# Kernel tuning notes

Hardware: AMD Instinct MI355X
Metric: run time of the kernel (lower is better)

## Reference

```python
import jax, jax.numpy as jnp
import numpy as np

TOKENS_PER_LAYER = 16  # v in rearrange 'b l (a v) -> b l a v'


def setup_inputs() -> dict:
    key = jax.random.key(0)
    k1, k2 = jax.random.split(key)
    vocab, embed_dim = 1024, 256
    x = jax.random.normal(k1, (64, 32, embed_dim * TOKENS_PER_LAYER), dtype=jnp.float32)
    # nn.Embedding init: uniform(-1/vocab, 1/vocab)
    emb_weight = jax.random.uniform(k2, (vocab, embed_dim), dtype=jnp.float32,
                                    minval=-1.0 / vocab, maxval=1.0 / vocab)
    return {"x": x, "emb_weight": emb_weight}


def reference(x, emb_weight):
    v = TOKENS_PER_LAYER
    b, l, av = x.shape
    a = av // v  # embed_dim
    # rearrange 'b l (a v) -> b l a v'
    z = x.reshape(b, l, a, v)
    # rearrange 'b l a v -> (b l v) a'
    z_flat = z.transpose(0, 1, 3, 2).reshape(b * l * v, a)
    # pairwise squared L2 distance via sum-of-squares + GEMM: [N, vocab]
    dist = (jnp.sum(z_flat * z_flat, axis=1, keepdims=True)
            + jnp.sum(emb_weight * emb_weight, axis=1)
            - 2.0 * (z_flat @ emb_weight.T))
    tokens = jnp.argmin(dist, axis=-1)  # [N] int
    # embedding gather, then rearrange '(b l v) e -> b l e v'
    z_q = emb_weight[tokens].reshape(b, l, v, a).transpose(0, 1, 3, 2)
    # straight-through decoder input: z + sg(z_q - z)
    decoder_input = z + jax.lax.stop_gradient(z_q - z)
    tokens = tokens.reshape(b, l, v)
    return z_q, decoder_input, tokens
```

## Files before the change

### kernel.cpp

```cpp
#include <hip/hip_runtime.h>


#define A_DIM 256
#define VOCAB 1024
#define NROWS 32768
#define ZQ_ELEMS ((size_t)8388608)
#define TAU_C 3.0e-4f
#define TAU_F 2.0e-4f

typedef _Float16 f16x8 __attribute__((ext_vector_type(8)));
typedef float f32x4 __attribute__((ext_vector_type(4)));

#define WS_EHT   ((size_t)0)
#define WS_ZH    ((size_t)524288)
#define WS_ESQ   ((size_t)17301504)
#define WS_ZSQ   ((size_t)17305600)
#define WS_QRES  ((size_t)17436672)
#define WS_TOK   ((size_t)20582400)
#define WS_PLIST ((size_t)20713472)
#define WS_FLIST ((size_t)21237760)
#define WS_CNT   ((size_t)21368832)
#define WS_NEED  ((size_t)21368960)

__device__ __forceinline__ void async_copy16(const void* g, void* l) {
    __builtin_amdgcn_global_load_lds(
        (const __attribute__((address_space(1))) unsigned int*)g,
        (__attribute__((address_space(3))) unsigned int*)l, 16, 0, 0);
}


__global__ __launch_bounds__(256) void prep_e_kernel(const float* __restrict__ emb,
                                                     float* __restrict__ esq,
                                                     _Float16* __restrict__ eht,
                                                     int* __restrict__ cnt) {
    int j = blockIdx.x * 256 + threadIdx.x;
    if (blockIdx.x == 0 && threadIdx.x < 2) cnt[threadIdx.x] = 0;
    if (j >= VOCAB) return;
    const float4* row = (const float4*)(emb + (size_t)j * A_DIM);
    double s = 0.0;
    #pragma unroll 4
    for (int t = 0; t < A_DIM / 4; ++t) {
        float4 f = row[t];
        float sx = f.x * f.x, sy = f.y * f.y, sz = f.z * f.z, sw = f.w * f.w;
        s += (double)sx + (double)sy + (double)sz + (double)sw;
    }
    esq[j] = (float)s;
    #pragma unroll 4
    for (int kb = 0; kb < 32; ++kb) {
        float4 e0 = row[kb * 2], e1 = row[kb * 2 + 1];
        f16x8 h;
        h[0] = (_Float16)e0.x; h[1] = (_Float16)e0.y; h[2] = (_Float16)e0.z; h[3] = (_Float16)e0.w;
        h[4] = (_Float16)e1.x; h[5] = (_Float16)e1.y; h[6] = (_Float16)e1.z; h[7] = (_Float16)e1.w;
        *(f16x8*)(eht + ((size_t)kb * 1024 + j) * 8) = h;
    }
}

__global__ __launch_bounds__(256) void prep_z_kernel(const float* __restrict__ x,
                                                     _Float16* __restrict__ zh,
                                                     float* __restrict__ zsq) {
    __shared__ float raw[A_DIM * 17];
    const int tid = threadIdx.x;
    const int bl = blockIdx.x;
    #pragma unroll
    for (int t = 0; t < 4; ++t) {
        int f4 = tid * 4 + t * 1024;
        float4 val = *(const float4*)(x + (size_t)bl * 4096 + f4);
        int a = f4 >> 4, v0 = f4 & 15;
        raw[a * 17 + v0 + 0] = val.x;
        raw[a * 17 + v0 + 1] = val.y;
        raw[a * 17 + v0 + 2] = val.z;
        raw[a * 17 + v0 + 3] = val.w;
    }
    __syncthreads();
    #pragma unroll
    for (int t = 0; t < 16; ++t) {
        int f = tid + t * 256;
        int v = f >> 8, a = f & 255;
        zh[((size_t)bl * 16 + v) * 256 + a] = (_Float16)raw[a * 17 + v];
    }
    if (tid < 16) {
        double s = 0.0;
        for (int a = 0; a < A_DIM; ++a) {
            float zf = raw[a * 17 + tid];
            float z2 = zf * zf;
            s += (double)z2;
        }
        zsq[bl * 16 + tid] = (float)s;
    }
}

__global__ __launch_bounds__(256, 4) void mfma_kernel(const _Float16* __restrict__ zh,
                                                      const _Float16* __restrict__ eht,
                                                      const float* __restrict__ esq_g,
                                                      float* __restrict__ qres) {
    __shared__ __align__(16) _Float16 lb[2][32 * 32 * 8];
    const int tid = threadIdx.x;
    const int w = tid >> 6;
    const int lane = tid & 63;
    const int q = lane >> 4;
    const int ln = lane & 15;

    const int wg = blockIdx.x;
    const int j = wg >> 3;
    const int rowblk = (wg & 7) * 64 + (j >> 2);
    const int quarter = j & 3;
    const int row0 = rowblk * 64 + w * 16;
    const int cq0 = quarter * 256;

    {
        #pragma unroll
        for (int t = 0; t < 4; ++t) {
            int f = tid + t * 256;
            const _Float16* gsrc = eht + ((size_t)(f >> 5) * 1024 + cq0 + (f & 31)) * 8;
            _Float16* ldst = &lb[0][(size_t)(t * 256 + w * 64) * 8];
            async_copy16(gsrc, ldst);
        }
    }

    f16x8 afr[8];
    #pragma unroll
    for (int kt = 0; kt < 8; ++kt)
        afr[kt] = *(const f16x8*)(zh + (size_t)(row0 + ln) * 256 + kt * 32 + q * 8);

    float tv1[4], tv2[4], tv3[4];
    int   ti1[4], ti2[4], ti3[4];
    #pragma unroll
    for (int s = 0; s < 4; ++s) {
        tv1[s] = 3.0e38f; tv2[s] = 3.0e38f; tv3[s] = 3.0e38f;
        ti1[s] = 0; ti2[s] = 0; ti3[s] = 0;
    }

    for (int chunk = 0; chunk < 8; ++chunk) {
        const int b = chunk & 1;
        asm volatile("s_waitcnt vmcnt(0)" ::: "memory");
        __syncthreads();
        if (chunk + 1 < 8) {
            const int cb = cq0 + (chunk + 1) * 32;
            #pragma unroll
            for (int t = 0; t < 4; ++t) {
                int f = tid + t * 256;
                const _Float16* gsrc = eht + ((size_t)(f >> 5) * 1024 + cb + (f & 31)) * 8;
                _Float16* ldst = &lb[b ^ 1][(size_t)(t * 256 + w * 64) * 8];
                async_copy16(gsrc, ldst);
            }
        }

        f32x4 acc[2];
        #pragma unroll
        for (int nt = 0; nt < 2; ++nt)
            acc[nt] = (f32x4){0.f, 0.f, 0.f, 0.f};

        #pragma unroll
        for (int kt = 0; kt < 8; ++kt) {
            #pragma unroll
            for (int nt = 0; nt < 2; ++nt) {
                f16x8 bfr = *(const f16x8*)&lb[b][((size_t)(kt * 4 + q) * 32 + nt * 16 + ln) * 8];
                acc[nt] = __builtin_amdgcn_mfma_f32_16x16x32_f16(afr[kt], bfr, acc[nt], 0, 0, 0);
            }
        }

        #pragma unroll
        for (int nt = 0; nt < 2; ++nt) {
            int c = cq0 + chunk * 32 + nt * 16 + ln;
            float es = esq_g[c];
            #pragma unroll
            for (int reg = 0; reg < 4; ++reg) {
                float s = fmaf(-2.0f, acc[nt][reg], es);
                if (s < tv3[reg]) {
                    if (s < tv2[reg]) {
                        tv3[reg] = tv2[reg]; ti3[reg] = ti2[reg];
                        if (s < tv1[reg]) {
                            tv2[reg] = tv1[reg]; ti2[reg] = ti1[reg];
                            tv1[reg] = s; ti1[reg] = c;
                        } else { tv2[reg] = s; ti2[reg] = c; }
                    } else { tv3[reg] = s; ti3[reg] = c; }
                }
            }
        }
    }

    #pragma unroll
    for (int slot = 0; slot < 4; ++slot) {
        float v1 = tv1[slot], v2 = tv2[slot], v3 = tv3[slot];
        int i1 = ti1[slot], i2 = ti2[slot], i3 = ti3[slot];
        #pragma unroll
        for (int m = 1; m <= 8; m <<= 1) {
            float ov1 = __shfl_xor(v1, m); int oi1 = __shfl_xor(i1, m);
            float ov2 = __shfl_xor(v2, m); int oi2 = __shfl_xor(i2, m);
            float ov3 = __shfl_xor(v3, m); int oi3 = __shfl_xor(i3, m);
            #define INS3(ov, oi)                                                         \
                if (ov < v3 || (ov == v3 && oi < i3)) {                                  \
                    if (ov < v2 || (ov == v2 && oi < i2)) {                              \
                        v3 = v2; i3 = i2;                                                \
                        if (ov < v1 || (ov == v1 && oi < i1)) {                          \
                            v2 = v1; i2 = i1; v1 = ov; i1 = oi;                          \
                        } else { v2 = ov; i2 = oi; }                                     \
                    } else { v3 = ov; i3 = oi; }                                         \
                }
            INS3(ov1, oi1)
            INS3(ov2, oi2)
            INS3(ov3, oi3)
            #undef INS3
        }
        if (ln == 0) {
            int row = row0 + q * 4 + slot;
            float* hp = qres + ((size_t)row * 4 + quarter) * 6;
            hp[0] = v1; hp[1] = __int_as_float(i1);
            hp[2] = v2; hp[3] = __int_as_float(i2);
            hp[4] = v3; hp[5] = __int_as_float(i3);
        }
    }
}

__global__ __launch_bounds__(256) void finalize_kernel(const float* __restrict__ qres,
                                                       int* __restrict__ tok,
                                                       int4* __restrict__ plist,
                                                       int* __restrict__ flist,
                                                       int* __restrict__ cnt,
                                                       float* __restrict__ out) {
    int row = blockIdx.x * 256 + threadIdx.x;
    const float* h0 = qres + (size_t)row * 24;
    float v1 = h0[0]; int i1 = __float_as_int(h0[1]);
    float v2 = h0[2]; int i2 = __float_as_int(h0[3]);
    float v3 = h0[4]; int i3 = __float_as_int(h0[5]);
    #pragma unroll
    for (int e = 0; e < 9; ++e) {
        float ov = h0[6 + 2 * e]; int oi = __float_as_int(h0[7 + 2 * e]);
        if (ov < v3 || (ov == v3 && oi < i3)) {
            if (ov < v2 || (ov == v2 && oi < i2)) {
                v3 = v2; i3 = i2;
                if (ov < v1 || (ov == v1 && oi < i1)) {
                    v2 = v1; i2 = i1; v1 = ov; i1 = oi;
                } else { v2 = ov; i2 = oi; }
            } else { v3 = ov; i3 = oi; }
        }
    }
    tok[row] = i1;
    out[2 * ZQ_ELEMS + (size_t)row] = (float)i1;
    if (v2 - v1 <= TAU_C) {
        if (v3 - v1 > TAU_C) {
            int p = atomicAdd(&cnt[0], 1);
            plist[p] = make_int4(row, i1, i2, 0);
        } else {
            int p = atomicAdd(&cnt[1], 1);
            flist[p] = row;
        }
    }
}

__global__ __launch_bounds__(256) void rescan2_kernel(const float* __restrict__ x,
                                                      const float* __restrict__ emb,
                                                      const float* __restrict__ esq,
                                                      const float* __restrict__ zsq,
                                                      int* __restrict__ tok,
                                                      const int4* __restrict__ plist,
                                                      const int* __restrict__ flist,
                                                      const int* __restrict__ cnt,
                                                      float* __restrict__ out) {
    __shared__ float zrow[A_DIM];
    __shared__ float wv[4];
    __shared__ int   wi[4];
    const int tid = threadIdx.x;
    const int w = tid >> 6, lane = tid & 63;

    {
        const int nw = gridDim.x * 4;
        const int gw = blockIdx.x * 4 + w;
        const int np = cnt[0];
        for (int i = gw; i < np; i += nw) {
            int4 e = plist[i];
            const int r = e.x, c1 = e.y, c2 = e.z;
            const float* xr = x + (size_t)(r >> 4) * 4096 + (r & 15);
            const float* e1 = emb + (size_t)c1 * A_DIM;
            const float* e2 = emb + (size_t)c2 * A_DIM;
            double d1 = 0.0, d2 = 0.0;
            #pragma unroll
            for (int k = 0; k < 4; ++k) {
                int a = lane + k * 64;
                double zv = (double)xr[a * 16];
                d1 = fma(zv, (double)e1[a], d1);
                d2 = fma(zv, (double)e2[a], d2);
            }
            #pragma unroll
            for (int m = 1; m < 64; m <<= 1) {
                d1 += __shfl_xor(d1, m);
                d2 += __shfl_xor(d2, m);
            }
            if (lane == 0) {
                float zq = zsq[r];
                float A1 = zq + esq[c1];
                float D1 = (float)(2.0 * d1);
                float s1 = A1 - D1;
                float A2 = zq + esq[c2];
                float D2 = (float)(2.0 * d2);
                float s2 = A2 - D2;
                int bi = (s2 < s1 || (s2 == s1 && c2 < c1)) ? c2 : c1;
                tok[r] = bi;
                out[2 * ZQ_ELEMS + (size_t)r] = (float)bi;
            }
        }
    }

    const int nf = cnt[1];
    for (int i = blockIdx.x; i < nf; i += gridDim.x) {
        const int r = flist[i];
        __syncthreads();
        zrow[tid] = x[(size_t)(r >> 4) * 4096 + (size_t)tid * 16 + (r & 15)];
        __syncthreads();

        const float4* e0 = (const float4*)(emb + (size_t)tid * 4 * A_DIM);
        double d0 = 0.0, d1 = 0.0, d2 = 0.0, d3 = 0.0;
        #pragma unroll 8
        for (int k4 = 0; k4 < A_DIM / 4; ++k4) {
            float4 zf = *(const float4*)&zrow[k4 * 4];
            double z0 = (double)zf.x, z1 = (double)zf.y;
            double z2 = (double)zf.z, z3 = (double)zf.w;
            float4 f0 = e0[k4];
            float4 f1 = e0[64 + k4];
            float4 f2 = e0[128 + k4];
            float4 f3 = e0[192 + k4];
            d0 = fma((double)f0.x, z0, d0); d0 = fma((double)f0.y, z1, d0);
            d0 = fma((double)f0.z, z2, d0); d0 = fma((double)f0.w, z3, d0);
            d1 = fma((double)f1.x, z0, d1); d1 = fma((double)f1.y, z1, d1);
            d1 = fma((double)f1.z, z2, d1); d1 = fma((double)f1.w, z3, d1);
            d2 = fma((double)f2.x, z0, d2); d2 = fma((double)f2.y, z1, d2);
            d2 = fma((double)f2.z, z2, d2); d2 = fma((double)f2.w, z3, d2);
            d3 = fma((double)f3.x, z0, d3); d3 = fma((double)f3.y, z1, d3);
            d3 = fma((double)f3.z, z2, d3); d3 = fma((double)f3.w, z3, d3);
        }
        const float zq = zsq[r];
        float bv = 3.0e38f; int bi = 0;
        double dd[4] = {d0, d1, d2, d3};
        #pragma unroll
        for (int cc = 0; cc < 4; ++cc) {
            int c = tid * 4 + cc;
            float A = zq + esq[c];
            float D = (float)(2.0 * dd[cc]);
            float s = A - D;
            if (s < bv) { bv = s; bi = c; }
        }
        #pragma unroll
        for (int m = 1; m < 64; m <<= 1) {
            float ov = __shfl_xor(bv, m); int oi = __shfl_xor(bi, m);
            if (ov < bv || (ov == bv && oi < bi)) { bv = ov; bi = oi; }
        }
        if (lane == 0) { wv[w] = bv; wi[w] = bi; }
        __syncthreads();
        if (tid == 0) {
            float BV = wv[0]; int BI = wi[0];
            #pragma unroll
            for (int t = 1; t < 4; ++t)
                if (wv[t] < BV || (wv[t] == BV && wi[t] < BI)) { BV = wv[t]; BI = wi[t]; }
            tok[r] = BI;
            out[2 * ZQ_ELEMS + (size_t)r] = (float)BI;
        }
    }
}

__global__ __launch_bounds__(256) void gather_kernel(const float* __restrict__ emb,
                                                     const int* __restrict__ tok,
                                                     float* __restrict__ out) {
    __shared__ int t16[16];
    const int tid = threadIdx.x;
    const int bl = blockIdx.x;
    if (tid < 16) t16[tid] = tok[bl * 16 + tid];
    __syncthreads();
    const int a = tid;
    __align__(16) float h[16];
    #pragma unroll
    for (int v = 0; v < 16; ++v) h[v] = emb[(size_t)t16[v] * A_DIM + a];
    size_t base = ((size_t)bl * A_DIM + a) * 16;
    float4* p0 = (float4*)(out + base);
    float4* p1 = (float4*)(out + ZQ_ELEMS + base);
    #pragma unroll
    for (int qq = 0; qq < 4; ++qq) {
        float4 val = *(float4*)&h[qq * 4];
        p0[qq] = val;
        p1[qq] = val;
    }
}


__global__ __launch_bounds__(256) void prep_f(const float* __restrict__ emb,
                                              float* __restrict__ e_sq32) {
    int j = blockIdx.x * 256 + threadIdx.x;
    if (j < VOCAB) {
        const float4* row = (const float4*)(emb + (size_t)j * A_DIM);
        double s = 0.0;
        #pragma unroll 4
        for (int t = 0; t < A_DIM / 4; ++t) {
            float4 f = row[t];
            float sx = f.x * f.x, sy = f.y * f.y, sz = f.z * f.z, sw = f.w * f.w;
            s += (double)sx + (double)sy + (double)sz + (double)sw;
        }
        e_sq32[j] = (float)s;
    }
}

#define FBM 64
#define FBN 256
#define FBK 32
struct SmemF {
    union {
        struct { float zs[FBK][FBM]; float es[FBK][FBN]; };
        float4 mbuf[FBM][32];
        struct { double zrow[A_DIM]; float rbest[256]; int ridx[256]; };
    };
    double zsqp_s[4][FBM];
    float  zsq[FBM];
    int    tok[FBM];
    int    flagrows[FBM];
    int    nflag;
};

__global__ __launch_bounds__(256, 2) void main_f(const float* __restrict__ x,
                                                 const float* __restrict__ emb,
                                                 const float* __restrict__ e_sq32,
                                                 float* __restrict__ out) {
    __shared__ SmemF sm;
    const int tid = threadIdx.x;
    const int tx = tid & 31;
    const int ty = tid >> 5;
    const int blk = blockIdx.x;
    const int row0 = blk * FBM;
    const int bl0 = row0 >> 4;
    const int zrow_id = tid & 63;
    const int zq4     = tid >> 6;

    if (tid == 0) sm.nflag = 0;
    float v1[8], v2[8];
    int   i1[8], i2[8];
    #pragma unroll
    for (int r = 0; r < 8; ++r) { v1[r] = 3.0e38f; v2[r] = 3.0e38f; i1[r] = 0; i2[r] = 0; }
    double zsqp = 0.0;
    float4 zpf[2];
    float4 epf[8];
    for (int ct = 0; ct < VOCAB / FBN; ++ct) {
        float acc[8][8];
        #pragma unroll
        for (int rr = 0; rr < 8; ++rr)
            #pragma unroll
            for (int cc = 0; cc < 8; ++cc) acc[rr][cc] = 0.0f;
        for (int kt = 0; kt < A_DIM / FBK; ++kt) {
            if (kt == 0) {
                #pragma unroll
                for (int t = 0; t < 2; ++t) {
                    int f = tid + t * 256;
                    int v4 = f & 3, g = (f >> 2) & 3, kk = f >> 4;
                    zpf[t] = *(const float4*)(x + (size_t)(bl0 + g) * 4096 + (kt * FBK + kk) * 16 + v4 * 4);
                }
                #pragma unroll
                for (int t = 0; t < 8; ++t) {
                    int f = tid + t * 256;
                    int c = f & 255, k4 = f >> 8;
                    epf[t] = *(const float4*)(emb + (size_t)(ct * FBN + c) * A_DIM + kt * FBK + k4 * 4);
                }
            }
            __syncthreads();
            #pragma unroll
            for (int t = 0; t < 2; ++t) {
                int f = tid + t * 256;
                int v4 = f & 3, g = (f >> 2) & 3, kk = f >> 4;
                *(float4*)&sm.zs[kk][g * 16 + v4 * 4] = zpf[t];
            }
            #pragma unroll
            for (int t = 0; t < 8; ++t) {
                int f = tid + t * 256;
                int c = f & 255, k4 = f >> 8;
                sm.es[k4 * 4 + 0][c] = epf[t].x;
                sm.es[k4 * 4 + 1][c] = epf[t].y;
                sm.es[k4 * 4 + 2][c] = epf[t].z;
                sm.es[k4 * 4 + 3][c] = epf[t].w;
            }
            __syncthreads();
            if (kt + 1 < A_DIM / FBK) {
                #pragma unroll
                for (int t = 0; t < 2; ++t) {
                    int f = tid + t * 256;
                    int v4 = f & 3, g = (f >> 2) & 3, kk = f >> 4;
                    zpf[t] = *(const float4*)(x + (size_t)(bl0 + g) * 4096 + ((kt + 1) * FBK + kk) * 16 + v4 * 4);
                }
                #pragma unroll
                for (int t = 0; t < 8; ++t) {
                    int f = tid + t * 256;
                    int c = f & 255, k4 = f >> 8;
                    epf[t] = *(const float4*)(emb + (size_t)(ct * FBN + c) * A_DIM + (kt + 1) * FBK + k4 * 4);
                }
            }
            if (ct == 0 && (kt >> 1) == zq4) {
                #pragma unroll
                for (int kk = 0; kk < FBK; ++kk) {
                    float zf = sm.zs[kk][zrow_id];
                    float zf2 = zf * zf;
                    zsqp += (double)zf2;
                }
            }
            #pragma unroll 2
            for (int kk = 0; kk < FBK; ++kk) {
                float4 za = *(float4*)&sm.zs[kk][ty * 4];
                float4 zb = *(float4*)&sm.zs[kk][32 + ty * 4];
                float4 ea = *(float4*)&sm.es[kk][tx * 4];
                float4 eb = *(float4*)&sm.es[kk][128 + tx * 4];
                float zv[8] = {za.x, za.y, za.z, za.w, zb.x, zb.y, zb.z, zb.w};
                float ev[8] = {ea.x, ea.y, ea.z, ea.w, eb.x, eb.y, eb.z, eb.w};
                #pragma unroll
                for (int rr = 0; rr < 8; ++rr)
                    #pragma unroll
                    for (int cc = 0; cc < 8; ++cc)
                        acc[rr][cc] = fmaf(zv[rr], ev[cc], acc[rr][cc]);
            }
        }
        if (ct == 0) {
            sm.zsqp_s[zq4][zrow_id] = zsqp;
            __syncthreads();
            if (tid < FBM)
                sm.zsq[tid] = (float)(sm.zsqp_s[0][tid] + sm.zsqp_s[1][tid]
                                    + sm.zsqp_s[2][tid] + sm.zsqp_s[3][tid]);
            __syncthreads();
        }
        float esqv[8];
        #pragma unroll
        for (int cc = 0; cc < 8; ++cc) {
            int c = ct * FBN + (cc >> 2) * 128 + tx * 4 + (cc & 3);
            esqv[cc] = e_sq32[c];
        }
        #pragma unroll
        for (int rr = 0; rr < 8; ++rr) {
            int R = (rr >> 2) * 32 + ty * 4 + (rr & 3);
            float zq = sm.zsq[R];
            #pragma unroll
            for (int cc = 0; cc < 8; ++cc) {
                int c = ct * FBN + (cc >> 2) * 128 + tx * 4 + (cc & 3);
                float A = zq + esqv[cc];
                float s = fmaf(-2.0f, acc[rr][cc], A);
                if (s < v1[rr]) { v2[rr] = v1[rr]; i2[rr] = i1[rr]; v1[rr] = s; i1[rr] = c; }
                else if (s < v2[rr]) { v2[rr] = s; i2[rr] = c; }
            }
        }
    }
    __syncthreads();
    #pragma unroll
    for (int rr = 0; rr < 8; ++rr) {
        int r = (rr >> 2) * 32 + ty * 4 + (rr & 3);
        float4 m;
        m.x = v1[rr]; m.y = __int_as_float(i1[rr]);
        m.z = v2[rr]; m.w = __int_as_float(i2[rr]);
        sm.mbuf[r][tx] = m;
    }
    __syncthreads();
    if (tid < FBM) {
        int r = tid;
        float V1 = 3.0e38f, V2 = 3.0e38f;
        int I1 = 0, I2 = 0;
        for (int t = 0; t < 32; ++t) {
            float4 m = sm.mbuf[r][t];
            float a1 = m.x; int a1i = __float_as_int(m.y);
            float a2 = m.z; int a2i = __float_as_int(m.w);
            if (a1 < V1 || (a1 == V1 && a1i < I1)) { V2 = V1; I2 = I1; V1 = a1; I1 = a1i; }
            else if (a1 < V2 || (a1 == V2 && a1i < I2)) { V2 = a1; I2 = a1i; }
            if (a2 < V1 || (a2 == V1 && a2i < I1)) { V2 = V1; I2 = I1; V1 = a2; I1 = a2i; }
            else if (a2 < V2 || (a2 == V2 && a2i < I2)) { V2 = a2; I2 = a2i; }
        }
        sm.tok[r] = I1;
        if (V2 - V1 <= TAU_F) {
            int pos = atomicAdd(&sm.nflag, 1);
            sm.flagrows[pos] = r;
        }
    }
    __syncthreads();
    const int nf = sm.nflag;
    for (int i = 0; i < nf; ++i) {
        const int rl = sm.flagrows[i];
        const int bl = bl0 + (rl >> 4);
        const int v  = rl & 15;
        const float zqrow = sm.zsq[rl];
        sm.zrow[tid] = (double)x[(size_t)bl * 4096 + (size_t)tid * 16 + v];
        __syncthreads();
        float bv = 3.0e38f; int bi = 0;
        #pragma unroll
        for (int cc = 0; cc < 4; ++cc) {
            int c = tid * 4 + cc;
            const float4* er = (const float4*)(emb + (size_t)c * A_DIM);
            double dot = 0.0;
            #pragma unroll 8
            for (int k4 = 0; k4 < A_DIM / 4; ++k4) {
                float4 f = er[k4];
                dot = fma((double)f.x, sm.zrow[k4 * 4 + 0], dot);
                dot = fma((double)f.y, sm.zrow[k4 * 4 + 1], dot);
                dot = fma((double)f.z, sm.zrow[k4 * 4 + 2], dot);
                dot = fma((double)f.w, sm.zrow[k4 * 4 + 3], dot);
            }
            float A = zqrow + e_sq32[c];
            float D = (float)(2.0 * dot);
            float s = A - D;
            if (s < bv) { bv = s; bi = c; }
        }
        sm.rbest[tid] = bv; sm.ridx[tid] = bi;
        __syncthreads();
        if (tid == 0) {
            float BV = sm.rbest[0]; int BI = sm.ridx[0];
            for (int t = 1; t < 256; ++t) {
                float vv = sm.rbest[t];
                if (vv < BV) { BV = vv; BI = sm.ridx[t]; }
            }
            sm.tok[rl] = BI;
        }
        __syncthreads();
    }
    if (tid < FBM) {
        out[2 * ZQ_ELEMS + (size_t)(row0 + tid)] = (float)sm.tok[tid];
    }
    __syncthreads();
    const int a = tid;
    for (int g = 0; g < 4; ++g) {
        __align__(16) float h[16];
        #pragma unroll
        for (int v = 0; v < 16; ++v) {
            h[v] = emb[(size_t)sm.tok[g * 16 + v] * A_DIM + a];
        }
        size_t base = ((size_t)(bl0 + g) * A_DIM + a) * 16;
        float4* p0 = (float4*)(out + base);
        float4* p1 = (float4*)(out + ZQ_ELEMS + base);
        #pragma unroll
        for (int qq = 0; qq < 4; ++qq) {
            float4 val = *(float4*)&h[qq * 4];
            p0[qq] = val;
            p1[qq] = val;
        }
    }
}

extern "C" void kernel_launch(void* const* d_in, const int* in_sizes, int n_in,
                              void* d_out, int out_size, void* d_ws, size_t ws_size,
                              hipStream_t stream) {
    (void)in_sizes; (void)n_in; (void)out_size;
    const float* x   = (const float*)d_in[0];
    const float* emb = (const float*)d_in[1];
    float* out = (float*)d_out;
    char* ws = (char*)d_ws;

    if (ws_size >= WS_NEED) {
        _Float16* eht = (_Float16*)(ws + WS_EHT);
        _Float16* zh  = (_Float16*)(ws + WS_ZH);
        float* esq    = (float*)(ws + WS_ESQ);
        float* zsq    = (float*)(ws + WS_ZSQ);
        float* qres   = (float*)(ws + WS_QRES);
        int* tok      = (int*)(ws + WS_TOK);
        int4* plist   = (int4*)(ws + WS_PLIST);
        int* flist    = (int*)(ws + WS_FLIST);
        int* cnt      = (int*)(ws + WS_CNT);

        prep_e_kernel<<<4, 256, 0, stream>>>(emb, esq, eht, cnt);
        prep_z_kernel<<<2048, 256, 0, stream>>>(x, zh, zsq);
        mfma_kernel<<<2048, 256, 0, stream>>>(zh, eht, esq, qres);
        finalize_kernel<<<128, 256, 0, stream>>>(qres, tok, plist, flist, cnt, out);
        rescan2_kernel<<<256, 256, 0, stream>>>(x, emb, esq, zsq, tok, plist, flist, cnt, out);
        gather_kernel<<<2048, 256, 0, stream>>>(emb, tok, out);
    } else {
        float* e_sq32 = (float*)ws;
        prep_f<<<4, 256, 0, stream>>>(emb, e_sq32);
        main_f<<<512, 256, 0, stream>>>(x, emb, e_sq32, out);
    }
}
```

Before: 250.5 us.

## Fuse finalize into MFMA kernel with full-vocab scan per block and register double-buffering

The MFMA kernel now scans all 1024 codebook entries per row block instead of splitting the vocabulary into quarters across blocks. It writes tokens and the ambiguous-row lists directly, which removes the partial-result buffer and the separate finalize kernel launch. B fragments are loaded straight from global memory into registers with two-way double buffering, replacing the LDS async-copy pipeline and its barriers. The trade-off is a grid of 512 blocks with lower occupancy (launch bounds 256,2) and a longer serial loop per wave, which may expose global load latency.

```diff
diff --git a/kernel.cpp b/kernel.cpp
--- a/kernel.cpp
+++ b/kernel.cpp
@@ -15,18 +15,11 @@
 #define WS_ZH    ((size_t)524288)
 #define WS_ESQ   ((size_t)17301504)
 #define WS_ZSQ   ((size_t)17305600)
-#define WS_QRES  ((size_t)17436672)
-#define WS_TOK   ((size_t)20582400)
-#define WS_PLIST ((size_t)20713472)
-#define WS_FLIST ((size_t)21237760)
-#define WS_CNT   ((size_t)21368832)
-#define WS_NEED  ((size_t)21368960)
-
-__device__ __forceinline__ void async_copy16(const void* g, void* l) {
-    __builtin_amdgcn_global_load_lds(
-        (const __attribute__((address_space(1))) unsigned int*)g,
-        (__attribute__((address_space(3))) unsigned int*)l, 16, 0, 0);
-}
+#define WS_TOK   ((size_t)17436672)
+#define WS_PLIST ((size_t)17567744)
+#define WS_FLIST ((size_t)18092032)
+#define WS_CNT   ((size_t)18223104)
+#define WS_NEED  ((size_t)18223232)
 
 
 __global__ __launch_bounds__(256) void prep_e_kernel(const float* __restrict__ emb,
@@ -89,33 +82,20 @@
     }
 }
 
-__global__ __launch_bounds__(256, 4) void mfma_kernel(const _Float16* __restrict__ zh,
+__global__ __launch_bounds__(256, 2) void mfma_kernel(const _Float16* __restrict__ zh,
                                                       const _Float16* __restrict__ eht,
                                                       const float* __restrict__ esq_g,
-                                                      float* __restrict__ qres) {
-    __shared__ __align__(16) _Float16 lb[2][32 * 32 * 8];
+                                                      int* __restrict__ tok,
+                                                      int4* __restrict__ plist,
+                                                      int* __restrict__ flist,
+                                                      int* __restrict__ cnt,
+                                                      float* __restrict__ out) {
     const int tid = threadIdx.x;
     const int w = tid >> 6;
     const int lane = tid & 63;
     const int q = lane >> 4;
     const int ln = lane & 15;
-
-    const int wg = blockIdx.x;
-    const int j = wg >> 3;
-    const int rowblk = (wg & 7) * 64 + (j >> 2);
-    const int quarter = j & 3;
-    const int row0 = rowblk * 64 + w * 16;
-    const int cq0 = quarter * 256;
-
-    {
-        #pragma unroll
-        for (int t = 0; t < 4; ++t) {
-            int f = tid + t * 256;
-            const _Float16* gsrc = eht + ((size_t)(f >> 5) * 1024 + cq0 + (f & 31)) * 8;
-            _Float16* ldst = &lb[0][(size_t)(t * 256 + w * 64) * 8];
-            async_copy16(gsrc, ldst);
-        }
-    }
+    const int row0 = blockIdx.x * 64 + w * 16;
 
     f16x8 afr[8];
     #pragma unroll
@@ -130,54 +110,48 @@
         ti1[s] = 0; ti2[s] = 0; ti3[s] = 0;
     }
 
-    for (int chunk = 0; chunk < 8; ++chunk) {
-        const int b = chunk & 1;
-        asm volatile("s_waitcnt vmcnt(0)" ::: "memory");
-        __syncthreads();
-        if (chunk + 1 < 8) {
-            const int cb = cq0 + (chunk + 1) * 32;
-            #pragma unroll
-            for (int t = 0; t < 4; ++t) {
-                int f = tid + t * 256;
-                const _Float16* gsrc = eht + ((size_t)(f >> 5) * 1024 + cb + (f & 31)) * 8;
-                _Float16* ldst = &lb[b ^ 1][(size_t)(t * 256 + w * 64) * 8];
-                async_copy16(gsrc, ldst);
-            }
-        }
-
-        f32x4 acc[2];
-        #pragma unroll
-        for (int nt = 0; nt < 2; ++nt)
-            acc[nt] = (f32x4){0.f, 0.f, 0.f, 0.f};
-
-        #pragma unroll
-        for (int kt = 0; kt < 8; ++kt) {
-            #pragma unroll
-            for (int nt = 0; nt < 2; ++nt) {
-                f16x8 bfr = *(const f16x8*)&lb[b][((size_t)(kt * 4 + q) * 32 + nt * 16 + ln) * 8];
-                acc[nt] = __builtin_amdgcn_mfma_f32_16x16x32_f16(afr[kt], bfr, acc[nt], 0, 0, 0);
-            }
-        }
-
-        #pragma unroll
-        for (int nt = 0; nt < 2; ++nt) {
-            int c = cq0 + chunk * 32 + nt * 16 + ln;
-            float es = esq_g[c];
-            #pragma unroll
-            for (int reg = 0; reg < 4; ++reg) {
-                float s = fmaf(-2.0f, acc[nt][reg], es);
-                if (s < tv3[reg]) {
-                    if (s < tv2[reg]) {
-                        tv3[reg] = tv2[reg]; ti3[reg] = ti2[reg];
-                        if (s < tv1[reg]) {
-                            tv2[reg] = tv1[reg]; ti2[reg] = ti1[reg];
-                            tv1[reg] = s; ti1[reg] = c;
-                        } else { tv2[reg] = s; ti2[reg] = c; }
-                    } else { tv3[reg] = s; ti3[reg] = c; }
-                }
-            }
-        }
-    }
+    #define LOAD_CHUNK(c0, bfr)                                                          \
+        {                                                                                \
+            _Pragma("unroll")                                                            \
+            for (int kt = 0; kt < 8; ++kt)                                               \
+                bfr[kt] = *(const f16x8*)(eht +                                          \
+                    ((size_t)(kt * 4 + q) * 1024 + (c0) + ln) * 8);                      \
+        }
+
+    #define COMPUTE_CHUNK(c0, bfr)                                                       \
+        {                                                                                \
+            f32x4 acc = (f32x4){0.f, 0.f, 0.f, 0.f};                                     \
+            _Pragma("unroll")                                                            \
+            for (int kt = 0; kt < 8; ++kt)                                               \
+                acc = __builtin_amdgcn_mfma_f32_16x16x32_f16(afr[kt], bfr[kt], acc,      \
+                                                             0, 0, 0);                   \
+            const int cand = (c0) + ln;                                                  \
+            float es = esq_g[cand];                                                      \
+            _Pragma("unroll")                                                            \
+            for (int reg = 0; reg < 4; ++reg) {                                          \
+                float s = fmaf(-2.0f, acc[reg], es);                                     \
+                if (s < tv3[reg]) {                                                      \
+                    if (s < tv2[reg]) {                                                  \
+                        tv3[reg] = tv2[reg]; ti3[reg] = ti2[reg];                        \
+                        if (s < tv1[reg]) {                                              \
+                            tv2[reg] = tv1[reg]; ti2[reg] = ti1[reg];                    \
+                            tv1[reg] = s; ti1[reg] = cand;                               \
+                        } else { tv2[reg] = s; ti2[reg] = cand; }                        \
+                    } else { tv3[reg] = s; ti3[reg] = cand; }                            \
+                }                                                                        \
+            }                                                                            \
+        }
+
+    f16x8 bA[8], bB[8];
+    LOAD_CHUNK(0, bA)
+    for (int ch = 0; ch < 64; ch += 2) {
+        LOAD_CHUNK((ch + 1) * 16, bB)
+        COMPUTE_CHUNK(ch * 16, bA)
+        if (ch + 2 < 64) LOAD_CHUNK((ch + 2) * 16, bA)
+        COMPUTE_CHUNK((ch + 1) * 16, bB)
+    }
+    #undef LOAD_CHUNK
+    #undef COMPUTE_CHUNK
 
     #pragma unroll
     for (int slot = 0; slot < 4; ++slot) {
@@ -204,46 +178,17 @@
         }
         if (ln == 0) {
             int row = row0 + q * 4 + slot;
-            float* hp = qres + ((size_t)row * 4 + quarter) * 6;
-            hp[0] = v1; hp[1] = __int_as_float(i1);
-            hp[2] = v2; hp[3] = __int_as_float(i2);
-            hp[4] = v3; hp[5] = __int_as_float(i3);
-        }
-    }
-}
-
-__global__ __launch_bounds__(256) void finalize_kernel(const float* __restrict__ qres,
-                                                       int* __restrict__ tok,
-                                                       int4* __restrict__ plist,
-                                                       int* __restrict__ flist,
-                                                       int* __restrict__ cnt,
-                                                       float* __restrict__ out) {
-    int row = blockIdx.x * 256 + threadIdx.x;
-    const float* h0 = qres + (size_t)row * 24;
-    float v1 = h0[0]; int i1 = __float_as_int(h0[1]);
-    float v2 = h0[2]; int i2 = __float_as_int(h0[3]);
-    float v3 = h0[4]; int i3 = __float_as_int(h0[5]);
-    #pragma unroll
-    for (int e = 0; e < 9; ++e) {
-        float ov = h0[6 + 2 * e]; int oi = __float_as_int(h0[7 + 2 * e]);
-        if (ov < v3 || (ov == v3 && oi < i3)) {
-            if (ov < v2 || (ov == v2 && oi < i2)) {
-                v3 = v2; i3 = i2;
-                if (ov < v1 || (ov == v1 && oi < i1)) {
-                    v2 = v1; i2 = i1; v1 = ov; i1 = oi;
-                } else { v2 = ov; i2 = oi; }
-            } else { v3 = ov; i3 = oi; }
-        }
-    }
-    tok[row] = i1;
-    out[2 * ZQ_ELEMS + (size_t)row] = (float)i1;
-    if (v2 - v1 <= TAU_C) {
-        if (v3 - v1 > TAU_C) {
-            int p = atomicAdd(&cnt[0], 1);
-            plist[p] = make_int4(row, i1, i2, 0);
-        } else {
-            int p = atomicAdd(&cnt[1], 1);
-            flist[p] = row;
+            tok[row] = i1;
+            out[2 * ZQ_ELEMS + (size_t)row] = (float)i1;
+            if (v2 - v1 <= TAU_C) {
+                if (v3 - v1 > TAU_C) {
+                    int p = atomicAdd(&cnt[0], 1) & (NROWS - 1);
+                    plist[p] = make_int4(row, i1, i2, 0);
+                } else {
+                    int p = atomicAdd(&cnt[1], 1) & (NROWS - 1);
+                    flist[p] = row;
+                }
+            }
         }
     }
 }
@@ -266,7 +211,7 @@
     {
         const int nw = gridDim.x * 4;
         const int gw = blockIdx.x * 4 + w;
-        const int np = cnt[0];
+        const int np = min(cnt[0], NROWS);
         for (int i = gw; i < np; i += nw) {
             int4 e = plist[i];
             const int r = e.x, c1 = e.y, c2 = e.z;
@@ -301,7 +246,7 @@
         }
     }
 
-    const int nf = cnt[1];
+    const int nf = min(cnt[1], NROWS);
     for (int i = blockIdx.x; i < nf; i += gridDim.x) {
         const int r = flist[i];
         __syncthreads();
@@ -644,7 +589,6 @@
         _Float16* zh  = (_Float16*)(ws + WS_ZH);
         float* esq    = (float*)(ws + WS_ESQ);
         float* zsq    = (float*)(ws + WS_ZSQ);
-        float* qres   = (float*)(ws + WS_QRES);
         int* tok      = (int*)(ws + WS_TOK);
         int4* plist   = (int4*)(ws + WS_PLIST);
         int* flist    = (int*)(ws + WS_FLIST);
@@ -652,8 +596,7 @@
 
         prep_e_kernel<<<4, 256, 0, stream>>>(emb, esq, eht, cnt);
         prep_z_kernel<<<2048, 256, 0, stream>>>(x, zh, zsq);
-        mfma_kernel<<<2048, 256, 0, stream>>>(zh, eht, esq, qres);
-        finalize_kernel<<<128, 256, 0, stream>>>(qres, tok, plist, flist, cnt, out);
+        mfma_kernel<<<512, 256, 0, stream>>>(zh, eht, esq, tok, plist, flist, cnt, out);
         rescan2_kernel<<<256, 256, 0, stream>>>(x, emb, esq, zsq, tok, plist, flist, cnt, out);
         gather_kernel<<<2048, 256, 0, stream>>>(emb, tok, out);
     } else {
```

After: 252.8 us. No clear change (+0.9%).
